# Kernel tuning notes

Measured on AMD Instinct MI355X. Metric: run time of the kernel, lower is better.

Reference implementation:

```python
import jax, jax.numpy as jnp
import numpy as np

D = 2048   # num_vars
H = 4096   # hidden width (2*D, pyro default)
B = 8192   # batch


def _made_masks():
    #   input degrees  : 1..D
    #   hidden degrees : arange(H) % (D-1) + 1  (in 1..D-1)
    #   output degrees : 1..D, strict inequality for the output layer
    inp_deg = np.arange(1, D + 1)
    hid_deg = np.arange(H) % (D - 1) + 1
    out_deg = np.arange(1, D + 1)
    m1 = (hid_deg[:, None] >= inp_deg[None, :]).astype(np.float32)  # [H, D]
    m2 = (hid_deg[:, None] >= hid_deg[None, :]).astype(np.float32)  # [H, H]
    m3 = (out_deg[:, None] > hid_deg[None, :]).astype(np.float32)   # [D, H]
    return jnp.asarray(m1), jnp.asarray(m2), jnp.asarray(m3)

M1, M2, M3 = _made_masks()
PERM = jnp.arange(D)  # permutation=torch.arange(num_vars) -> identity gather


def setup_inputs() -> dict:
    key = jax.random.key(0)
    ks = jax.random.split(key, 7)
    value = jax.random.randint(ks[0], (B, D), 0, 2).astype(jnp.float32)
    s1 = 1.0 / np.sqrt(D)
    s2 = 1.0 / np.sqrt(H)
    W1 = jax.random.uniform(ks[1], (H, D), minval=-s1, maxval=s1, dtype=jnp.float32)
    b1 = jax.random.uniform(ks[2], (H,), minval=-s1, maxval=s1, dtype=jnp.float32)
    W2 = jax.random.uniform(ks[3], (H, H), minval=-s2, maxval=s2, dtype=jnp.float32)
    b2 = jax.random.uniform(ks[4], (H,), minval=-s2, maxval=s2, dtype=jnp.float32)
    W3 = jax.random.uniform(ks[5], (D, H), minval=-s2, maxval=s2, dtype=jnp.float32)
    b3 = jax.random.uniform(ks[6], (D,), minval=-s2, maxval=s2, dtype=jnp.float32)
    return {"value": value, "W1": W1, "b1": b1, "W2": W2, "b2": b2,
            "W3": W3, "b3": b3}


def reference(value, W1, b1, W2, b2, W3, b3):
    h1 = jax.nn.relu(value @ (W1 * M1).T + b1)          # [B, H]
    h2 = jax.nn.relu(h1 @ (W2 * M2).T + b2)             # [B, H]
    logits = h2 @ (W3 * M3).T + b3                      # [B, D]
    logits = logits[:, PERM]                            # identity permutation gather
    # Bernoulli(logits).log_prob(value) = value*logits - softplus(logits)
    log_prob = (value * logits - jax.nn.softplus(logits)).sum(axis=1)  # [B]
    return log_prob
```

## Files before the change

kernel.cpp:

```cpp
#include <hip/hip_runtime.h>
#include <hip/hip_bf16.h>
#include <cstdint>

typedef short short8 __attribute__((ext_vector_type(8)));
typedef float floatx4 __attribute__((ext_vector_type(4)));
typedef float f32x4 __attribute__((ext_vector_type(4)));
typedef unsigned short u16;
typedef unsigned short u16x4 __attribute__((ext_vector_type(4)));

#define BB 8192
#define DD 2048
#define HH 4096

static __device__ __forceinline__ u16 f2bf(float x) {
  __hip_bfloat16 h = __float2bfloat16(x);
  return __builtin_bit_cast(u16, h);
}

static __device__ __forceinline__ float bf2f(u16 x) {
  unsigned int u = ((unsigned int)x) << 16;
  return __builtin_bit_cast(float, u);
}

static __device__ __forceinline__ void glds16(const u16* g, u16* l) {
  __builtin_amdgcn_global_load_lds(
      (const __attribute__((address_space(1))) void*)g,
      (__attribute__((address_space(3))) void*)l, 16, 0, 0);
}

__global__ void cvt_value_kernel(const float* __restrict__ in, u16* __restrict__ out, int n4) {
  int idx = blockIdx.x * blockDim.x + threadIdx.x;
  int stride = gridDim.x * blockDim.x;
  for (int i = idx; i < n4; i += stride) {
    f32x4 v = reinterpret_cast<const f32x4*>(in)[i];
    u16x4 o = { f2bf(v[0]), f2bf(v[1]), f2bf(v[2]), f2bf(v[3]) };
    reinterpret_cast<u16x4*>(out)[i] = o;
  }
}

template<int MODE>
__global__ __launch_bounds__(256) void mask_cvt_tile(const float* __restrict__ in,
                                                     u16* __restrict__ out, int W) {
  const int r0 = blockIdx.y * 64;
  const int c0 = blockIdx.x * 64;
  const int re = r0 + 63, ce = c0 + 63;

  bool zero;
  if (MODE == 0) {
    int rmaxd = (r0 >= 2047) ? ((re <= 4093) ? (re - 2047) : 2046)
                             : ((re <= 2046) ? re : 2046);
    zero = (c0 > rmaxd);
  } else if (MODE == 1) {
    int rmaxd = (r0 >= 2047) ? ((re <= 4093) ? (re - 2047) : 2046)
                             : ((re <= 2046) ? re : 2046);
    int cmind = (c0 >= 2047) ? ((ce >= 4094) ? 0 : (c0 - 2047))
                             : ((ce >= 2047) ? 0 : c0);
    zero = (cmind > rmaxd);
  } else {
    int cmind = (c0 >= 2047) ? ((ce >= 4094) ? 0 : (c0 - 2047))
                             : ((ce >= 2047) ? 0 : c0);
    zero = (re <= cmind);
  }

  const int tr = threadIdx.x >> 4;
  const int tc = (threadIdx.x & 15) * 4;

  if (zero) {
    u16x4 z = {0, 0, 0, 0};
#pragma unroll
    for (int rr = 0; rr < 64; rr += 16)
      *(u16x4*)&out[(size_t)(r0 + tr + rr) * W + c0 + tc] = z;
    return;
  }

#pragma unroll
  for (int rr = 0; rr < 64; rr += 16) {
    int r = r0 + tr + rr;
    int rdeg = r % 2047;
    f32x4 v = *(const f32x4*)&in[(size_t)r * W + c0 + tc];
    u16x4 o;
#pragma unroll
    for (int e = 0; e < 4; ++e) {
      int c = c0 + tc + e;
      bool keep;
      if (MODE == 0)      keep = (c <= rdeg);
      else if (MODE == 1) keep = ((c % 2047) <= rdeg);
      else                keep = (r > (c % 2047));
      o[e] = keep ? f2bf(v[e]) : (u16)0;
    }
    *(u16x4*)&out[(size_t)r * W + c0 + tc] = o;
  }
}

template<int MASKM>
__global__ __launch_bounds__(512, 2) void gemm256_kernel(
    const u16* __restrict__ A, const u16* __restrict__ Bw,
    const float* __restrict__ bias, u16* __restrict__ C,
    int M, int N, int K)
{
  __shared__ u16 ls[2][32768];

  const int tid  = threadIdx.x;
  const int wid  = tid >> 6;
  const int lane = tid & 63;
  const int wm = wid >> 2, wn = wid & 3;
  const int l15 = lane & 15, lhi = lane >> 4;
  const int brow = blockIdx.y * 256;
  const int p = blockIdx.x;
  int cols[2];
  cols[0] = (p < 4) ? p : p + 4;
  cols[1] = (p < 4) ? 7 - p : 19 - p;

  const int arow_ = tid >> 3;
  const int agsub = (tid & 7) ^ (arow_ & 7);
  size_t aB[4];
  aB[0] = (size_t)(brow +   0 + arow_) * K + agsub * 8;
  aB[1] = (size_t)(brow + 128 + arow_) * K + agsub * 8;
  aB[2] = (size_t)(brow +  64 + arow_) * K + agsub * 8;
  aB[3] = (size_t)(brow + 192 + arow_) * K + agsub * 8;
  const int aCh[4] = {0, 1024, 512, 1536};

#pragma unroll 1
  for (int t = 0; t < 2; ++t) {
    const int bcol = cols[t] * 256;

    int rmax;
    {
      int sC = bcol, e = bcol + 255;
      if (e <= 2046)       rmax = e;
      else if (sC <= 2046) rmax = 2046;
      else { int em = e - 2047; rmax = (em <= 2046) ? em : 2046; }
    }
    int r1end = ((rmax >> 6) + 1) << 6; if (r1end > K) r1end = K;
    int run2start, r2end;
    if (MASKM == 1) { run2start = r1end; r2end = r1end; }
    else {
      run2start = (1984 > r1end) ? 1984 : r1end;
      r2end = (((2047 + rmax) >> 6) + 1) << 6; if (r2end > K) r2end = K;
      if (r2end < run2start) r2end = run2start;
    }
    const int n1 = r1end >> 6;
    const int nt = n1 + ((r2end - run2start) >> 6);
    const int roff = run2start - r1end;
    const int nte = nt + ((MASKM != 1 && r2end < K) ? 1 : 0);

    size_t bB[2][2];
#pragma unroll
    for (int u = 0; u < 2; ++u)
#pragma unroll
      for (int c = 0; c < 2; ++c)
        bB[u][c] = (size_t)(bcol + u * 128 + arow_ + 64 * c) * K + agsub * 8;

    floatx4 acc[8][4];
#pragma unroll
    for (int i = 0; i < 8; ++i)
#pragma unroll
      for (int j = 0; j < 4; ++j)
        acc[i][j] = (floatx4){0.f, 0.f, 0.f, 0.f};

#define K0F(j) (((j) >= nt) ? (K - 64) : (((j) << 6) + (((j) >= n1) ? roff : 0)))
#define ST_A(slot_, idx_, k0v) glds16(A + aB[idx_] + (k0v), (u16*)&ls[slot_][(aCh[idx_] + tid) * 8])
#define ST_B(slot_, u_, k0v) do { \
      glds16(Bw + bB[u_][0] + (k0v), (u16*)&ls[slot_][(2048 + (u_) * 1024 + tid) * 8]); \
      glds16(Bw + bB[u_][1] + (k0v), (u16*)&ls[slot_][(2048 + (u_) * 1024 + tid + 512) * 8]); \
    } while (0)

    ST_A(0, 0, K0F(0)); ST_A(0, 1, K0F(0));
    ST_B(0, 0, K0F(0)); ST_B(0, 1, K0F(0));
    ST_A(0, 2, K0F(0)); ST_A(0, 3, K0F(0));
    if (nte > 1) {
      const int k1p = K0F(1);
      ST_A(1, 0, k1p); ST_A(1, 1, k1p);
      asm volatile("s_waitcnt vmcnt(4)" ::: "memory");
    } else {
      asm volatile("s_waitcnt vmcnt(2)" ::: "memory");
    }
    __builtin_amdgcn_sched_barrier(0);
    __builtin_amdgcn_s_barrier();

#pragma unroll 1
    for (int i = 0; i < nte; ++i) {
      const int s = i & 1, o = s ^ 1;
      const u16* sA = &ls[s][0];
      const u16* sB = &ls[s][16384];
      const bool g1 = (i + 1 < nte), g2 = (i + 2 < nte);
      const int k1 = g1 ? K0F(i + 1) : 0;
      const int k2 = g2 ? K0F(i + 2) : 0;
      short8 af[4], bf0[4], bf1[4];

#define RD_A(q_, ks_) do { \
        _Pragma("unroll") \
        for (int mi = 0; mi < 4; ++mi) { \
          int row = wm * 128 + (q_) * 64 + mi * 16 + l15; \
          int ch = row * 8 + (((ks_) * 4 + lhi) ^ (row & 7)); \
          af[mi] = *(const short8*)&sA[ch * 8]; \
        } } while (0)
#define RD_B(ks_, dst_) do { \
        _Pragma("unroll") \
        for (int ni = 0; ni < 4; ++ni) { \
          int row = wn * 64 + ni * 16 + l15; \
          int ch = row * 8 + (((ks_) * 4 + lhi) ^ (row & 7)); \
          dst_[ni] = *(const short8*)&sB[ch * 8]; \
        } } while (0)
#define MFMA16(q_, bf_) do { \
        _Pragma("unroll") \
        for (int mi = 0; mi < 4; ++mi) \
          _Pragma("unroll") \
          for (int ni = 0; ni < 4; ++ni) \
            acc[(q_) * 4 + mi][ni] = __builtin_amdgcn_mfma_f32_16x16x32_bf16( \
                af[mi], bf_[ni], acc[(q_) * 4 + mi][ni], 0, 0, 0); \
        } while (0)

      RD_A(0, 0);
      RD_B(0, bf0);
      if (g1) ST_B(o, 0, k1);
      __builtin_amdgcn_s_barrier();
      asm volatile("s_waitcnt lgkmcnt(0)" ::: "memory");
      __builtin_amdgcn_sched_barrier(0);
      __builtin_amdgcn_s_setprio(1);
      MFMA16(0, bf0);
      __builtin_amdgcn_s_setprio(0);
      __builtin_amdgcn_s_barrier();

      RD_A(0, 1);
      RD_B(1, bf1);
      if (g1) ST_B(o, 1, k1);
      __builtin_amdgcn_s_barrier();
      asm volatile("s_waitcnt lgkmcnt(0)" ::: "memory");
      __builtin_amdgcn_sched_barrier(0);
      __builtin_amdgcn_s_setprio(1);
      MFMA16(0, bf1);
      __builtin_amdgcn_s_setprio(0);
      if (g1) {
        if (i == 0) asm volatile("s_waitcnt vmcnt(6)" ::: "memory");
        else        asm volatile("s_waitcnt vmcnt(5)" ::: "memory");
      } else {
        asm volatile("s_waitcnt vmcnt(0)" ::: "memory");
      }
      __builtin_amdgcn_sched_barrier(0);
      __builtin_amdgcn_s_barrier();

      RD_A(1, 0);
      if (g1) ST_A(o, 2, k1);
      if (g2) ST_A(s, 0, k2);
      __builtin_amdgcn_s_barrier();
      asm volatile("s_waitcnt lgkmcnt(0)" ::: "memory");
      __builtin_amdgcn_sched_barrier(0);
      __builtin_amdgcn_s_setprio(1);
      MFMA16(1, bf0);
      __builtin_amdgcn_s_setprio(0);
      __builtin_amdgcn_s_barrier();

      RD_A(1, 1);
      if (g1) ST_A(o, 3, k1);
      if (g2) ST_A(s, 1, k2);
      __builtin_amdgcn_s_barrier();
      asm volatile("s_waitcnt lgkmcnt(0)" ::: "memory");
      __builtin_amdgcn_sched_barrier(0);
      __builtin_amdgcn_s_setprio(1);
      MFMA16(1, bf1);
      __builtin_amdgcn_s_setprio(0);
      if (g1) {
        if (g2) asm volatile("s_waitcnt vmcnt(4)" ::: "memory");
        else    asm volatile("s_waitcnt vmcnt(2)" ::: "memory");
        __builtin_amdgcn_sched_barrier(0);
      }
      __builtin_amdgcn_s_barrier();
#undef RD_A
#undef RD_B
#undef MFMA16
    }

#pragma unroll
    for (int mi = 0; mi < 8; ++mi) {
      int row = brow + wm * 128 + (mi >> 2) * 64 + (mi & 3) * 16 + lhi * 4;
#pragma unroll
      for (int ni = 0; ni < 4; ++ni) {
        int col = bcol + wn * 64 + ni * 16 + l15;
        float bv = bias[col];
#pragma unroll
        for (int e = 0; e < 4; ++e) {
          float v = acc[mi][ni][e] + bv;
          v = fmaxf(v, 0.0f);
          C[(size_t)(row + e) * N + col] = f2bf(v);
        }
      }
    }
    __syncthreads();
#undef K0F
#undef ST_A
#undef ST_B
  }
}

__global__ __launch_bounds__(512, 1) void gemm3p_kernel(
    const u16* __restrict__ A,
    const u16* __restrict__ Bw,
    const float* __restrict__ bias,
    const u16* __restrict__ vbf,
    float* __restrict__ outp,
    int M, int N, int K)
{
  __shared__ u16 ls[2][24576];

  const int tid  = threadIdx.x;
  const int wid  = tid >> 6;
  const int lane = tid & 63;
  const int wm = wid >> 2, wn = wid & 3;
  const int l15 = lane & 15, lhi = lane >> 4;
  const int brow = blockIdx.y * 128;
  const int q = blockIdx.x;
  int sgs[2] = { q, 7 - q };

  size_t aOff[2];
#pragma unroll
  for (int u = 0; u < 2; ++u) {
    int ch = tid + 512 * u;
    int row = ch >> 3, sub = ch & 7;
    aOff[u] = (size_t)(brow + row) * K + (sub ^ (row & 7)) * 8;
  }
  int bRow[4], bSsub[4];
#pragma unroll
  for (int u = 0; u < 4; ++u) {
    int ch = tid + 512 * u;
    bRow[u] = ch >> 3;
    bSsub[u] = (ch & 7) ^ (bRow[u] & 7);
  }

#pragma unroll 1
  for (int t = 0; t < 2; ++t) {
    const int bcol = sgs[t] * 256;
    const int rmax = bcol + 254;

    int r1end = ((rmax >> 6) + 1) << 6; if (r1end > K) r1end = K;
    int run2start = (1984 > r1end) ? 1984 : r1end;
    int r2end = (((2047 + rmax) >> 6) + 1) << 6; if (r2end > K) r2end = K;
    if (r2end < run2start) r2end = run2start;
    const int n1 = r1end >> 6;
    const int nt = n1 + ((r2end - run2start) >> 6);
    const int roff = run2start - r1end;
    const int nte = nt + ((r2end < K) ? 1 : 0);

    size_t bOff[4];
#pragma unroll
    for (int u = 0; u < 4; ++u)
      bOff[u] = (size_t)(bcol + bRow[u]) * K + bSsub[u] * 8;

    floatx4 acc[4][4];
#pragma unroll
    for (int i = 0; i < 4; ++i)
#pragma unroll
      for (int j = 0; j < 4; ++j)
        acc[i][j] = (floatx4){0.f, 0.f, 0.f, 0.f};

#define K0G(j) (((j) >= nt) ? (K - 64) : (((j) << 6) + (((j) >= n1) ? roff : 0)))
#define ST3(slot_, k0v) do { \
      glds16(A  + aOff[0] + (k0v), (u16*)&ls[slot_][tid * 8]); \
      glds16(A  + aOff[1] + (k0v), (u16*)&ls[slot_][(512 + tid) * 8]); \
      glds16(Bw + bOff[0] + (k0v), (u16*)&ls[slot_][(1024 + tid) * 8]); \
      glds16(Bw + bOff[1] + (k0v), (u16*)&ls[slot_][(1536 + tid) * 8]); \
      glds16(Bw + bOff[2] + (k0v), (u16*)&ls[slot_][(2048 + tid) * 8]); \
      glds16(Bw + bOff[3] + (k0v), (u16*)&ls[slot_][(2560 + tid) * 8]); \
    } while (0)

    ST3(0, K0G(0));
    asm volatile("s_waitcnt vmcnt(0)" ::: "memory");
    __builtin_amdgcn_sched_barrier(0);
    __builtin_amdgcn_s_barrier();

#pragma unroll 1
    for (int i = 0; i < nte; ++i) {
      const int s = i & 1, o = s ^ 1;
      const u16* sA = &ls[s][0];
      const u16* sB = &ls[s][8192];
      const bool g1 = (i + 1 < nte);
      short8 af[4], bfv[4];

#pragma unroll
      for (int mi = 0; mi < 4; ++mi) {
        int row = wm * 64 + mi * 16 + l15;
        af[mi] = *(const short8*)&sA[(row * 8 + (lhi ^ (row & 7))) * 8];
      }
#pragma unroll
      for (int ni = 0; ni < 4; ++ni) {
        int row = wn * 64 + ni * 16 + l15;
        bfv[ni] = *(const short8*)&sB[(row * 8 + (lhi ^ (row & 7))) * 8];
      }
      if (g1) ST3(o, K0G(i + 1));
      __builtin_amdgcn_s_barrier();
      asm volatile("s_waitcnt lgkmcnt(0)" ::: "memory");
      __builtin_amdgcn_sched_barrier(0);
      __builtin_amdgcn_s_setprio(1);
#pragma unroll
      for (int mi = 0; mi < 4; ++mi)
#pragma unroll
        for (int ni = 0; ni < 4; ++ni)
          acc[mi][ni] = __builtin_amdgcn_mfma_f32_16x16x32_bf16(af[mi], bfv[ni], acc[mi][ni], 0, 0, 0);
      __builtin_amdgcn_s_setprio(0);
      __builtin_amdgcn_s_barrier();

#pragma unroll
      for (int mi = 0; mi < 4; ++mi) {
        int row = wm * 64 + mi * 16 + l15;
        af[mi] = *(const short8*)&sA[(row * 8 + ((4 + lhi) ^ (row & 7))) * 8];
      }
#pragma unroll
      for (int ni = 0; ni < 4; ++ni) {
        int row = wn * 64 + ni * 16 + l15;
        bfv[ni] = *(const short8*)&sB[(row * 8 + ((4 + lhi) ^ (row & 7))) * 8];
      }
      __builtin_amdgcn_s_barrier();
      asm volatile("s_waitcnt lgkmcnt(0)" ::: "memory");
      __builtin_amdgcn_sched_barrier(0);
      __builtin_amdgcn_s_setprio(1);
#pragma unroll
      for (int mi = 0; mi < 4; ++mi)
#pragma unroll
        for (int ni = 0; ni < 4; ++ni)
          acc[mi][ni] = __builtin_amdgcn_mfma_f32_16x16x32_bf16(af[mi], bfv[ni], acc[mi][ni], 0, 0, 0);
      __builtin_amdgcn_s_setprio(0);
      if (g1) {
        asm volatile("s_waitcnt vmcnt(0)" ::: "memory");
        __builtin_amdgcn_sched_barrier(0);
      }
      __builtin_amdgcn_s_barrier();
    }
#undef K0G
#undef ST3

#pragma unroll
    for (int mi = 0; mi < 4; ++mi) {
#pragma unroll
      for (int e = 0; e < 4; ++e) {
        int row = brow + wm * 64 + mi * 16 + lhi * 4 + e;
        float partial = 0.0f;
#pragma unroll
        for (int ni = 0; ni < 4; ++ni) {
          int col = bcol + wn * 64 + ni * 16 + l15;
          float l = acc[mi][ni][e] + bias[col];
          float v = bf2f(vbf[(size_t)row * N + col]);
          float sp = fmaxf(l, 0.0f) + __logf(1.0f + __expf(-fabsf(l)));
          partial += v * l - sp;
        }
#pragma unroll
        for (int off = 1; off < 16; off <<= 1)
          partial += __shfl_xor(partial, off, 64);
        if (l15 == 0) atomicAdd(&outp[row], partial);
      }
    }
  }
}

extern "C" void kernel_launch(void* const* d_in, const int* in_sizes, int n_in,
                              void* d_out, int out_size, void* d_ws, size_t ws_size,
                              hipStream_t stream) {
  const float* value = (const float*)d_in[0];
  const float* W1 = (const float*)d_in[1];
  const float* b1 = (const float*)d_in[2];
  const float* W2 = (const float*)d_in[3];
  const float* b2 = (const float*)d_in[4];
  const float* W3 = (const float*)d_in[5];
  const float* b3 = (const float*)d_in[6];
  float* out = (float*)d_out;

  char* ws = (char*)d_ws;
  u16* vbf = (u16*)(ws);
  u16* w1m = (u16*)(ws + 33554432ULL);
  u16* w2m = (u16*)(ws + 50331648ULL);
  u16* w3m = (u16*)(ws + 83886080ULL);
  u16* h1  = (u16*)(ws + 100663296ULL);
  u16* h2  = (u16*)(ws + 167772160ULL);

  hipMemsetAsync(d_out, 0, (size_t)out_size * sizeof(float), stream);

  cvt_value_kernel<<<2048, 256, 0, stream>>>(value, vbf, (BB * DD) / 4);
  mask_cvt_tile<0><<<dim3(DD / 64, HH / 64), 256, 0, stream>>>(W1, w1m, DD);
  mask_cvt_tile<1><<<dim3(HH / 64, HH / 64), 256, 0, stream>>>(W2, w2m, HH);
  mask_cvt_tile<2><<<dim3(HH / 64, DD / 64), 256, 0, stream>>>(W3, w3m, HH);

  dim3 g12(8, BB / 256);
  gemm256_kernel<1><<<g12, 512, 0, stream>>>(vbf, w1m, b1, h1, BB, HH, DD);
  gemm256_kernel<2><<<g12, 512, 0, stream>>>(h1, w2m, b2, h2, BB, HH, HH);
  dim3 g3(4, BB / 128);
  gemm3p_kernel<<<g3, 512, 0, stream>>>(h2, w3m, b3, vbf, out, BB, DD, HH);
}
```

Before: 395.6 us.

## Simplify GEMM pipelines to issue full next-tile prefetch up front with one barrier

Replaces the finely interleaved multi-phase prefetch schedule (staggered A/B stores across sub-steps, deeper lookahead, many s_barriers, and tuned vmcnt waits) with a simple double-buffer. The whole next tile is issued at the top of each iteration, and there is a single vmcnt(0) wait plus barrier at the end. It applies to both the hidden-layer GEMM and the output GEMM. This removes most per-iteration workgroup barriers, but it loses the two-tile lookahead and the overlap of loads with finer-grained phases, which can expose global latency.

```diff
diff --git a/kernel.cpp b/kernel.cpp
--- a/kernel.cpp
+++ b/kernel.cpp
@@ -164,29 +164,32 @@
       glds16(Bw + bB[u_][0] + (k0v), (u16*)&ls[slot_][(2048 + (u_) * 1024 + tid) * 8]); \
       glds16(Bw + bB[u_][1] + (k0v), (u16*)&ls[slot_][(2048 + (u_) * 1024 + tid + 512) * 8]); \
     } while (0)
-
-    ST_A(0, 0, K0F(0)); ST_A(0, 1, K0F(0));
-    ST_B(0, 0, K0F(0)); ST_B(0, 1, K0F(0));
-    ST_A(0, 2, K0F(0)); ST_A(0, 3, K0F(0));
-    if (nte > 1) {
-      const int k1p = K0F(1);
-      ST_A(1, 0, k1p); ST_A(1, 1, k1p);
-      asm volatile("s_waitcnt vmcnt(4)" ::: "memory");
-    } else {
-      asm volatile("s_waitcnt vmcnt(2)" ::: "memory");
-    }
+#define ST_TILE(slot_, k0v) do { \
+      ST_A(slot_, 0, k0v); ST_A(slot_, 1, k0v); ST_A(slot_, 2, k0v); ST_A(slot_, 3, k0v); \
+      ST_B(slot_, 0, k0v); ST_B(slot_, 1, k0v); \
+    } while (0)
+
+    {
+      const int k00 = K0F(0);
+      ST_TILE(0, k00);
+    }
+    asm volatile("s_waitcnt vmcnt(0)" ::: "memory");
     __builtin_amdgcn_sched_barrier(0);
     __builtin_amdgcn_s_barrier();
+    __builtin_amdgcn_sched_barrier(0);
 
 #pragma unroll 1
     for (int i = 0; i < nte; ++i) {
       const int s = i & 1, o = s ^ 1;
       const u16* sA = &ls[s][0];
       const u16* sB = &ls[s][16384];
-      const bool g1 = (i + 1 < nte), g2 = (i + 2 < nte);
-      const int k1 = g1 ? K0F(i + 1) : 0;
-      const int k2 = g2 ? K0F(i + 2) : 0;
+      const bool g1 = (i + 1 < nte);
       short8 af[4], bf0[4], bf1[4];
+
+      if (g1) {
+        const int k1 = K0F(i + 1);
+        ST_TILE(o, k1);
+      }
 
 #define RD_A(q_, ks_) do { \
         _Pragma("unroll") \
@@ -213,59 +216,38 @@
 
       RD_A(0, 0);
       RD_B(0, bf0);
-      if (g1) ST_B(o, 0, k1);
-      __builtin_amdgcn_s_barrier();
       asm volatile("s_waitcnt lgkmcnt(0)" ::: "memory");
       __builtin_amdgcn_sched_barrier(0);
       __builtin_amdgcn_s_setprio(1);
       MFMA16(0, bf0);
       __builtin_amdgcn_s_setprio(0);
-      __builtin_amdgcn_s_barrier();
 
       RD_A(0, 1);
       RD_B(1, bf1);
-      if (g1) ST_B(o, 1, k1);
+      asm volatile("s_waitcnt lgkmcnt(0)" ::: "memory");
+      __builtin_amdgcn_sched_barrier(0);
+      __builtin_amdgcn_s_setprio(1);
+      MFMA16(0, bf1);
+      __builtin_amdgcn_s_setprio(0);
+
+      RD_A(1, 0);
+      asm volatile("s_waitcnt lgkmcnt(0)" ::: "memory");
+      __builtin_amdgcn_sched_barrier(0);
+      __builtin_amdgcn_s_setprio(1);
+      MFMA16(1, bf0);
+      __builtin_amdgcn_s_setprio(0);
+
+      RD_A(1, 1);
+      asm volatile("s_waitcnt lgkmcnt(0)" ::: "memory");
+      __builtin_amdgcn_sched_barrier(0);
+      __builtin_amdgcn_s_setprio(1);
+      MFMA16(1, bf1);
+      __builtin_amdgcn_s_setprio(0);
+
+      asm volatile("s_waitcnt vmcnt(0)" ::: "memory");
+      __builtin_amdgcn_sched_barrier(0);
       __builtin_amdgcn_s_barrier();
-      asm volatile("s_waitcnt lgkmcnt(0)" ::: "memory");
-      __builtin_amdgcn_sched_barrier(0);
-      __builtin_amdgcn_s_setprio(1);
-      MFMA16(0, bf1);
-      __builtin_amdgcn_s_setprio(0);
-      if (g1) {
-        if (i == 0) asm volatile("s_waitcnt vmcnt(6)" ::: "memory");
-        else        asm volatile("s_waitcnt vmcnt(5)" ::: "memory");
-      } else {
-        asm volatile("s_waitcnt vmcnt(0)" ::: "memory");
-      }
-      __builtin_amdgcn_sched_barrier(0);
-      __builtin_amdgcn_s_barrier();
-
-      RD_A(1, 0);
-      if (g1) ST_A(o, 2, k1);
-      if (g2) ST_A(s, 0, k2);
-      __builtin_amdgcn_s_barrier();
-      asm volatile("s_waitcnt lgkmcnt(0)" ::: "memory");
-      __builtin_amdgcn_sched_barrier(0);
-      __builtin_amdgcn_s_setprio(1);
-      MFMA16(1, bf0);
-      __builtin_amdgcn_s_setprio(0);
-      __builtin_amdgcn_s_barrier();
-
-      RD_A(1, 1);
-      if (g1) ST_A(o, 3, k1);
-      if (g2) ST_A(s, 1, k2);
-      __builtin_amdgcn_s_barrier();
-      asm volatile("s_waitcnt lgkmcnt(0)" ::: "memory");
-      __builtin_amdgcn_sched_barrier(0);
-      __builtin_amdgcn_s_setprio(1);
-      MFMA16(1, bf1);
-      __builtin_amdgcn_s_setprio(0);
-      if (g1) {
-        if (g2) asm volatile("s_waitcnt vmcnt(4)" ::: "memory");
-        else    asm volatile("s_waitcnt vmcnt(2)" ::: "memory");
-        __builtin_amdgcn_sched_barrier(0);
-      }
-      __builtin_amdgcn_s_barrier();
+      __builtin_amdgcn_sched_barrier(0);
 #undef RD_A
 #undef RD_B
 #undef MFMA16
@@ -290,6 +272,7 @@
 #undef K0F
 #undef ST_A
 #undef ST_B
+#undef ST_TILE
   }
 }
 
@@ -367,6 +350,7 @@
     asm volatile("s_waitcnt vmcnt(0)" ::: "memory");
     __builtin_amdgcn_sched_barrier(0);
     __builtin_amdgcn_s_barrier();
+    __builtin_amdgcn_sched_barrier(0);
 
 #pragma unroll 1
     for (int i = 0; i < nte; ++i) {
@@ -376,6 +360,8 @@
       const bool g1 = (i + 1 < nte);
       short8 af[4], bfv[4];
 
+      if (g1) ST3(o, K0G(i + 1));
+
 #pragma unroll
       for (int mi = 0; mi < 4; ++mi) {
         int row = wm * 64 + mi * 16 + l15;
@@ -386,8 +372,6 @@
         int row = wn * 64 + ni * 16 + l15;
         bfv[ni] = *(const short8*)&sB[(row * 8 + (lhi ^ (row & 7))) * 8];
       }
-      if (g1) ST3(o, K0G(i + 1));
-      __builtin_amdgcn_s_barrier();
       asm volatile("s_waitcnt lgkmcnt(0)" ::: "memory");
       __builtin_amdgcn_sched_barrier(0);
       __builtin_amdgcn_s_setprio(1);
@@ -397,7 +381,6 @@
         for (int ni = 0; ni < 4; ++ni)
           acc[mi][ni] = __builtin_amdgcn_mfma_f32_16x16x32_bf16(af[mi], bfv[ni], acc[mi][ni], 0, 0, 0);
       __builtin_amdgcn_s_setprio(0);
-      __builtin_amdgcn_s_barrier();
 
 #pragma unroll
       for (int mi = 0; mi < 4; ++mi) {
@@ -409,7 +392,6 @@
         int row = wn * 64 + ni * 16 + l15;
         bfv[ni] = *(const short8*)&sB[(row * 8 + ((4 + lhi) ^ (row & 7))) * 8];
       }
-      __builtin_amdgcn_s_barrier();
       asm volatile("s_waitcnt lgkmcnt(0)" ::: "memory");
       __builtin_amdgcn_sched_barrier(0);
       __builtin_amdgcn_s_setprio(1);
@@ -419,11 +401,11 @@
         for (int ni = 0; ni < 4; ++ni)
           acc[mi][ni] = __builtin_amdgcn_mfma_f32_16x16x32_bf16(af[mi], bfv[ni], acc[mi][ni], 0, 0, 0);
       __builtin_amdgcn_s_setprio(0);
-      if (g1) {
-        asm volatile("s_waitcnt vmcnt(0)" ::: "memory");
-        __builtin_amdgcn_sched_barrier(0);
-      }
+
+      asm volatile("s_waitcnt vmcnt(0)" ::: "memory");
+      __builtin_amdgcn_sched_barrier(0);
       __builtin_amdgcn_s_barrier();
+      __builtin_amdgcn_sched_barrier(0);
     }
 #undef K0G
 #undef ST3
```

After: 387.4 us. 2.1% less time.
